# Kernel tuning notes

Hardware: AMD Instinct MI355X
Metric: run time of the kernel (lower is better)

## Reference

```python
import jax, jax.numpy as jnp
import numpy as np

IN_DIM, OUT_DIM = 256, 64
ALPHA = 0.2  # leaky relu negative slope
NEG_INF = -1e30


def setup_inputs() -> dict:
    key = jax.random.key(0)
    k1, k2, k3, k4 = jax.random.split(key, 4)
    B, N = 8, 2048
    h = jax.random.normal(k1, (B, N, IN_DIM), dtype=jnp.float32)
    adj = jax.random.randint(k2, (B, N, N), 0, 2, dtype=jnp.int32)
    # ensure no fully-isolated node (avoids softmax over all -inf)
    idx = jnp.arange(N)
    adj = adj.at[:, idx, idx].set(1)
    # params: fc.weight [out,in] -> store transposed [in,out]; attn_fc.weight [1, 2*out] -> [2*out]
    W = jax.random.normal(k3, (IN_DIM, OUT_DIM), dtype=jnp.float32) / np.sqrt(IN_DIM)
    a = jax.random.normal(k4, (2 * OUT_DIM,), dtype=jnp.float32) / np.sqrt(2 * OUT_DIM)
    return {"h": h, "adj": adj, "W": W, "a": a}


def reference(h, adj, W, a):
    # Wh: [B,N,D]
    Wh = jnp.einsum("bni,io->bno", h, W)
    D = Wh.shape[-1]
    # concat-based additive attention decomposed: e[b,i,j] = lrelu(a1.Wh_i + a2.Wh_j)
    a1, a2 = a[:D], a[D:]
    s1 = Wh @ a1  # [B,N] contribution of row node i
    s2 = Wh @ a2  # [B,N] contribution of col node j
    e = jax.nn.leaky_relu(s1[:, :, None] + s2[:, None, :], negative_slope=ALPHA)  # [B,N,N]
    e = jnp.where(adj == 0, NEG_INF, e)
    attn = jax.nn.softmax(e, axis=-1)
    # dropout is identity in eval mode
    return jnp.einsum("bij,bjd->bid", attn, Wh)
```

## Files before the change

### kernel.cpp

```cpp
#include <hip/hip_runtime.h>
#include <math.h>

#define NB 8
#define NN 2048
#define IN_DIM 256
#define OUT_DIM 64
#define ALPHA 0.2f
#define JSPLIT 8

typedef __attribute__((ext_vector_type(8))) short bf16x8;
typedef __attribute__((ext_vector_type(4))) float f32x4;
typedef __attribute__((ext_vector_type(4))) int i32x4;

__device__ __forceinline__ unsigned short f2bf(float x) {
    union { float f; unsigned u; } v; v.f = x;
    unsigned r = v.u + 0x7FFF + ((v.u >> 16) & 1);
    return (unsigned short)(r >> 16);
}

__device__ __forceinline__ unsigned cvt_pk_bf16(float lo, float hi) {
    unsigned r;
    asm("v_cvt_pk_bf16_f32 %0, %1, %2" : "=v"(r) : "v"(lo), "v"(hi));
    return r;
}

#define WT_STRIDE 264
__global__ __launch_bounds__(256) void wh_kernel(const float* __restrict__ h,
                                                 const float* __restrict__ W,
                                                 const float* __restrict__ a,
                                                 unsigned short* __restrict__ Whbt,
                                                 float* __restrict__ s1,
                                                 float* __restrict__ s2) {
    __shared__ unsigned short Wt[OUT_DIM * WT_STRIDE];
    const int t = threadIdx.x;

    #pragma unroll 8
    for (int rep = 0; rep < 64; ++rep) {
        const int id = rep * 256 + t;
        const int k = id >> 6, n = id & 63;
        Wt[n * WT_STRIDE + k] = f2bf(W[id]);
    }
    __syncthreads();

    const int lane = t & 63, wv = t >> 6;
    const int m = lane & 15, quad = lane >> 4;
    const long gr0 = (long)(blockIdx.x * 4 + wv) * 16;

    f32x4 acc[4];
    #pragma unroll
    for (int nt = 0; nt < 4; ++nt) acc[nt] = (f32x4){0.f, 0.f, 0.f, 0.f};

    #pragma unroll
    for (int ks = 0; ks < 8; ++ks) {
        const int k0 = ks * 32;
        const float* hp = h + (gr0 + m) * IN_DIM + k0 + quad * 8;
        const float4 ha = *(const float4*)hp;
        const float4 hb = *(const float4*)(hp + 4);
        union { bf16x8 v; unsigned u32[4]; } af;
        af.u32[0] = cvt_pk_bf16(ha.x, ha.y);
        af.u32[1] = cvt_pk_bf16(ha.z, ha.w);
        af.u32[2] = cvt_pk_bf16(hb.x, hb.y);
        af.u32[3] = cvt_pk_bf16(hb.z, hb.w);
        #pragma unroll
        for (int nt = 0; nt < 4; ++nt) {
            const bf16x8 bf_ = *(const bf16x8*)(const void*)
                &Wt[(nt * 16 + m) * WT_STRIDE + k0 + quad * 8];
            acc[nt] = __builtin_amdgcn_mfma_f32_16x16x32_bf16(af.v, bf_, acc[nt], 0, 0, 0);
        }
    }

    const int b  = (int)(gr0 >> 11);
    const int ib = (int)(gr0 & 2047);

    #pragma unroll
    for (int nt = 0; nt < 4; ++nt) {
        ushort4 w4;
        w4.x = f2bf(acc[nt][0]); w4.y = f2bf(acc[nt][1]);
        w4.z = f2bf(acc[nt][2]); w4.w = f2bf(acc[nt][3]);
        *(ushort4*)&Whbt[((long)(b * OUT_DIM + nt * 16 + m) << 11) + ib + quad * 4] = w4;
    }

    float a1v[4], a2v[4];
    #pragma unroll
    for (int nt = 0; nt < 4; ++nt) {
        a1v[nt] = a[nt * 16 + m];
        a2v[nt] = a[OUT_DIM + nt * 16 + m];
    }
    #pragma unroll
    for (int reg = 0; reg < 4; ++reg) {
        float p1 = 0.f, p2 = 0.f;
        #pragma unroll
        for (int nt = 0; nt < 4; ++nt) {
            p1 += acc[nt][reg] * a1v[nt];
            p2 += acc[nt][reg] * a2v[nt];
        }
        #pragma unroll
        for (int off = 1; off < 16; off <<= 1) {
            p1 += __shfl_xor(p1, off, 64);
            p2 += __shfl_xor(p2, off, 64);
        }
        if (m == 0) {
            s1[gr0 + quad * 4 + reg] = p1;
            s2[gr0 + quad * 4 + reg] = p2;
        }
    }
}

__global__ __launch_bounds__(256) void attn_kernel(const int* __restrict__ adj,
                                                   const unsigned short* __restrict__ Whbt,
                                                   const float* __restrict__ s1,
                                                   const float* __restrict__ s2,
                                                   float* __restrict__ part,
                                                   float* __restrict__ lpart) {
    const int t = threadIdx.x, lane = t & 63, wv = t >> 6;

    const int bid = blockIdx.x;
    const int js  = bid & (JSPLIT - 1);
    const int itg = (bid >> 3) & 31;
    const int b   = bid >> 8;
    const int i0  = itg * 64 + wv * 16;
    const int jlo = js * (NN / JSPLIT);

    const int m = lane & 15, quad = lane >> 4;

    const float s1v = s1[b * NN + i0 + m];

    f32x4 acc[4];
    #pragma unroll
    for (int nt = 0; nt < 4; ++nt) acc[nt] = (f32x4){0.f, 0.f, 0.f, 0.f};
    float lacc = 0.f;

    const int* adjp = adj + (long)b * NN * NN + (long)(i0 + m) * NN + jlo + quad * 8;
    const float* s2p = s2 + b * NN + jlo + quad * 8;
    const unsigned short* wbase = Whbt + ((long)(b * OUT_DIM) << 11) + jlo + quad * 8;

    i32x4 av0 = __builtin_nontemporal_load((const i32x4*)adjp);
    i32x4 av1 = __builtin_nontemporal_load((const i32x4*)(adjp + 4));
    f32x4 sv0 = *(const f32x4*)s2p;
    f32x4 sv1 = *(const f32x4*)(s2p + 4);

    const int NSTEP = NN / JSPLIT / 32;
    for (int ks = 0; ks < NSTEP; ++ks) {
        const int j0 = ks * 32;

        bf16x8 bfr[4];
        #pragma unroll
        for (int nt = 0; nt < 4; ++nt)
            bfr[nt] = *(const bf16x8*)(const void*)
                &wbase[((long)(nt * 16 + m) << 11) + j0];

        const i32x4 a0 = av0, a1 = av1;
        const f32x4 t0 = sv0, t1 = sv1;
        const int jn = (ks + 1 < NSTEP) ? j0 + 32 : j0;
        av0 = __builtin_nontemporal_load((const i32x4*)(adjp + jn));
        av1 = __builtin_nontemporal_load((const i32x4*)(adjp + jn + 4));
        sv0 = *(const f32x4*)(s2p + jn);
        sv1 = *(const f32x4*)(s2p + jn + 4);

        float p[8];
        #pragma unroll
        for (int u = 0; u < 4; ++u) {
            float e = s1v + t0[u];
            e = fmaxf(e, ALPHA * e);
            const float ex = __expf(e);
            p[u] = (a0[u] != 0) ? ex : 0.f;
        }
        #pragma unroll
        for (int u = 0; u < 4; ++u) {
            float e = s1v + t1[u];
            e = fmaxf(e, ALPHA * e);
            const float ex = __expf(e);
            p[4 + u] = (a1[u] != 0) ? ex : 0.f;
        }
        lacc += ((p[0] + p[1]) + (p[2] + p[3])) + ((p[4] + p[5]) + (p[6] + p[7]));

        union { bf16x8 v; unsigned u32[4]; } af;
        af.u32[0] = cvt_pk_bf16(p[0], p[1]);
        af.u32[1] = cvt_pk_bf16(p[2], p[3]);
        af.u32[2] = cvt_pk_bf16(p[4], p[5]);
        af.u32[3] = cvt_pk_bf16(p[6], p[7]);

        #pragma unroll
        for (int nt = 0; nt < 4; ++nt)
            acc[nt] = __builtin_amdgcn_mfma_f32_16x16x32_bf16(af.v, bfr[nt], acc[nt], 0, 0, 0);
    }

    lacc += __shfl_xor(lacc, 16, 64);
    lacc += __shfl_xor(lacc, 32, 64);
    if (quad == 0)
        lpart[js * (NB * NN) + b * NN + i0 + m] = lacc;

    float* pp = part + (long)js * ((long)NB * NN * OUT_DIM)
                     + ((long)(b * NN + i0) << 6);
    #pragma unroll
    for (int nt = 0; nt < 4; ++nt)
        #pragma unroll
        for (int reg = 0; reg < 4; ++reg)
            pp[(quad * 4 + reg) * OUT_DIM + nt * 16 + m] = acc[nt][reg];
}

__global__ __launch_bounds__(256) void finalize_kernel(const float* __restrict__ part,
                                                       const float* __restrict__ lpart,
                                                       float* __restrict__ out) {
    const int idx = blockIdx.x * 256 + threadIdx.x;
    const int row = idx >> 4;
    float l = 0.f;
    #pragma unroll
    for (int s = 0; s < JSPLIT; ++s) l += lpart[s * (NB * NN) + row];
    float4 v = make_float4(0.f, 0.f, 0.f, 0.f);
    const float4* p4 = (const float4*)part;
    #pragma unroll
    for (int s = 0; s < JSPLIT; ++s) {
        const float4 p = p4[(long)s * ((long)NB * NN * OUT_DIM / 4) + idx];
        v.x += p.x; v.y += p.y; v.z += p.z; v.w += p.w;
    }
    const float inv = 1.f / l;
    v.x *= inv; v.y *= inv; v.z *= inv; v.w *= inv;
    ((float4*)out)[idx] = v;
}

extern "C" void kernel_launch(void* const* d_in, const int* in_sizes, int n_in,
                              void* d_out, int out_size, void* d_ws, size_t ws_size,
                              hipStream_t stream) {
    const float* h   = (const float*)d_in[0];
    const int*   adj = (const int*)d_in[1];
    const float* W   = (const float*)d_in[2];
    const float* a   = (const float*)d_in[3];
    float* out = (float*)d_out;

    float* s1    = (float*)d_ws;
    float* s2    = s1 + NB * NN;
    float* lpart = s2 + NB * NN;
    float* part  = lpart + JSPLIT * NB * NN;
    unsigned short* Whbt = (unsigned short*)(part + (long)JSPLIT * NB * NN * OUT_DIM);

    wh_kernel<<<NB * NN / 64, 256, 0, stream>>>(h, W, a, Whbt, s1, s2);
    attn_kernel<<<NB * (NN / 64) * JSPLIT, 256, 0, stream>>>(adj, Whbt, s1, s2, part, lpart);
    finalize_kernel<<<NB * NN * OUT_DIM / 4 / 256, 256, 0, stream>>>(part, lpart, out);
}
```

Before: 244.0 us.

## Pack adjacency into bitmask in separate pass, halve j-split, prefetch Wh fragments

```diff
diff --git a/kernel.cpp b/kernel.cpp
--- a/kernel.cpp
+++ b/kernel.cpp
@@ -6,11 +6,12 @@
 #define IN_DIM 256
 #define OUT_DIM 64
 #define ALPHA 0.2f
-#define JSPLIT 8
+#define JSPLIT 4
 
 typedef __attribute__((ext_vector_type(8))) short bf16x8;
 typedef __attribute__((ext_vector_type(4))) float f32x4;
 typedef __attribute__((ext_vector_type(4))) int i32x4;
+typedef __attribute__((ext_vector_type(4))) unsigned u32x4;
 
 __device__ __forceinline__ unsigned short f2bf(float x) {
     union { float f; unsigned u; } v; v.f = x;
@@ -22,6 +23,23 @@
     unsigned r;
     asm("v_cvt_pk_bf16_f32 %0, %1, %2" : "=v"(r) : "v"(lo), "v"(hi));
     return r;
+}
+
+__global__ __launch_bounds__(256) void pack_kernel(const int* __restrict__ adj,
+                                                   unsigned* __restrict__ mask) {
+    const int t = threadIdx.x, lane = t & 63, wv = t >> 6;
+    const int r = blockIdx.x * 4 + wv;
+    const int* ap = adj + (long)r * NN + lane * 32;
+    unsigned bits = 0;
+    #pragma unroll
+    for (int u = 0; u < 8; ++u) {
+        const i32x4 v = __builtin_nontemporal_load((const i32x4*)(ap + 4 * u));
+        bits |= (unsigned)(v[0] & 1) << (4 * u + 0);
+        bits |= (unsigned)(v[1] & 1) << (4 * u + 1);
+        bits |= (unsigned)(v[2] & 1) << (4 * u + 2);
+        bits |= (unsigned)(v[3] & 1) << (4 * u + 3);
+    }
+    mask[r * 64 + lane] = bits;
 }
 
 #define WT_STRIDE 264
@@ -106,7 +124,7 @@
     }
 }
 
-__global__ __launch_bounds__(256) void attn_kernel(const int* __restrict__ adj,
+__global__ __launch_bounds__(256) void attn_kernel(const unsigned* __restrict__ mask,
                                                    const unsigned short* __restrict__ Whbt,
                                                    const float* __restrict__ s1,
                                                    const float* __restrict__ s2,
@@ -116,8 +134,8 @@
 
     const int bid = blockIdx.x;
     const int js  = bid & (JSPLIT - 1);
-    const int itg = (bid >> 3) & 31;
-    const int b   = bid >> 8;
+    const int itg = (bid >> 2) & 31;
+    const int b   = bid >> 7;
     const int i0  = itg * 64 + wv * 16;
     const int jlo = js * (NN / JSPLIT);
 
@@ -125,52 +143,54 @@
 
     const float s1v = s1[b * NN + i0 + m];
 
+    const unsigned* mrowp = mask + ((long)(b * NN + i0 + m) << 6) + (js << 4);
+    u32x4 md[4];
+    #pragma unroll
+    for (int d = 0; d < 4; ++d) md[d] = *(const u32x4*)(mrowp + 4 * d);
+
     f32x4 acc[4];
     #pragma unroll
     for (int nt = 0; nt < 4; ++nt) acc[nt] = (f32x4){0.f, 0.f, 0.f, 0.f};
     float lacc = 0.f;
 
-    const int* adjp = adj + (long)b * NN * NN + (long)(i0 + m) * NN + jlo + quad * 8;
     const float* s2p = s2 + b * NN + jlo + quad * 8;
     const unsigned short* wbase = Whbt + ((long)(b * OUT_DIM) << 11) + jlo + quad * 8;
 
-    i32x4 av0 = __builtin_nontemporal_load((const i32x4*)adjp);
-    i32x4 av1 = __builtin_nontemporal_load((const i32x4*)(adjp + 4));
     f32x4 sv0 = *(const f32x4*)s2p;
     f32x4 sv1 = *(const f32x4*)(s2p + 4);
+    bf16x8 bn[4];
+    #pragma unroll
+    for (int nt = 0; nt < 4; ++nt)
+        bn[nt] = *(const bf16x8*)(const void*)&wbase[(long)(nt * 16 + m) << 11];
 
     const int NSTEP = NN / JSPLIT / 32;
+    #pragma unroll
     for (int ks = 0; ks < NSTEP; ++ks) {
         const int j0 = ks * 32;
-
-        bf16x8 bfr[4];
-        #pragma unroll
-        for (int nt = 0; nt < 4; ++nt)
-            bfr[nt] = *(const bf16x8*)(const void*)
-                &wbase[((long)(nt * 16 + m) << 11) + j0];
-
-        const i32x4 a0 = av0, a1 = av1;
+        const int jn = (ks + 1 < NSTEP) ? j0 + 32 : j0;
+
         const f32x4 t0 = sv0, t1 = sv1;
-        const int jn = (ks + 1 < NSTEP) ? j0 + 32 : j0;
-        av0 = __builtin_nontemporal_load((const i32x4*)(adjp + jn));
-        av1 = __builtin_nontemporal_load((const i32x4*)(adjp + jn + 4));
+        bf16x8 bc[4];
+        #pragma unroll
+        for (int nt = 0; nt < 4; ++nt) bc[nt] = bn[nt];
+
         sv0 = *(const f32x4*)(s2p + jn);
         sv1 = *(const f32x4*)(s2p + jn + 4);
+        #pragma unroll
+        for (int nt = 0; nt < 4; ++nt)
+            bn[nt] = *(const bf16x8*)(const void*)
+                &wbase[((long)(nt * 16 + m) << 11) + jn];
+
+        const unsigned mdw  = md[ks >> 2][ks & 3];
+        const unsigned byte8 = (mdw >> (quad * 8)) & 0xffu;
 
         float p[8];
         #pragma unroll
-        for (int u = 0; u < 4; ++u) {
-            float e = s1v + t0[u];
+        for (int u = 0; u < 8; ++u) {
+            float e = s1v + (u < 4 ? t0[u] : t1[u - 4]);
             e = fmaxf(e, ALPHA * e);
             const float ex = __expf(e);
-            p[u] = (a0[u] != 0) ? ex : 0.f;
-        }
-        #pragma unroll
-        for (int u = 0; u < 4; ++u) {
-            float e = s1v + t1[u];
-            e = fmaxf(e, ALPHA * e);
-            const float ex = __expf(e);
-            p[4 + u] = (a1[u] != 0) ? ex : 0.f;
+            p[u] = ((byte8 >> u) & 1u) ? ex : 0.f;
         }
         lacc += ((p[0] + p[1]) + (p[2] + p[3])) + ((p[4] + p[5]) + (p[6] + p[7]));
 
@@ -182,7 +202,7 @@
 
         #pragma unroll
         for (int nt = 0; nt < 4; ++nt)
-            acc[nt] = __builtin_amdgcn_mfma_f32_16x16x32_bf16(af.v, bfr[nt], acc[nt], 0, 0, 0);
+            acc[nt] = __builtin_amdgcn_mfma_f32_16x16x32_bf16(af.v, bc[nt], acc[nt], 0, 0, 0);
     }
 
     lacc += __shfl_xor(lacc, 16, 64);
@@ -233,8 +253,10 @@
     float* lpart = s2 + NB * NN;
     float* part  = lpart + JSPLIT * NB * NN;
     unsigned short* Whbt = (unsigned short*)(part + (long)JSPLIT * NB * NN * OUT_DIM);
-
+    unsigned* mask = (unsigned*)(Whbt + (long)NB * OUT_DIM * NN);
+
+    pack_kernel<<<NB * NN / 4, 256, 0, stream>>>(adj, mask);
     wh_kernel<<<NB * NN / 64, 256, 0, stream>>>(h, W, a, Whbt, s1, s2);
-    attn_kernel<<<NB * (NN / 64) * JSPLIT, 256, 0, stream>>>(adj, Whbt, s1, s2, part, lpart);
+    attn_kernel<<<NB * (NN / 64) * JSPLIT, 256, 0, stream>>>(mask, Whbt, s1, s2, part, lpart);
     finalize_kernel<<<NB * NN * OUT_DIM / 4 / 256, 256, 0, stream>>>(part, lpart, out);
 }
```

Result: slower. 272.1 us (+11.5%).

## Fuse split-J reduction into attention kernel via LDS, drop finalize kernel

Applied to the files above, without the earlier changes.

```diff
diff --git a/kernel.cpp b/kernel.cpp
--- a/kernel.cpp
+++ b/kernel.cpp
@@ -6,7 +6,6 @@
 #define IN_DIM 256
 #define OUT_DIM 64
 #define ALPHA 0.2f
-#define JSPLIT 8
 
 typedef __attribute__((ext_vector_type(8))) short bf16x8;
 typedef __attribute__((ext_vector_type(4))) float f32x4;
@@ -106,20 +105,20 @@
     }
 }
 
+#define AB_STRIDE 68
 __global__ __launch_bounds__(256) void attn_kernel(const int* __restrict__ adj,
                                                    const unsigned short* __restrict__ Whbt,
                                                    const float* __restrict__ s1,
                                                    const float* __restrict__ s2,
-                                                   float* __restrict__ part,
-                                                   float* __restrict__ lpart) {
+                                                   float* __restrict__ out) {
+    __shared__ float accbuf[4][16 * AB_STRIDE];
+    __shared__ float l_lds[4][16];
+
     const int t = threadIdx.x, lane = t & 63, wv = t >> 6;
-
     const int bid = blockIdx.x;
-    const int js  = bid & (JSPLIT - 1);
-    const int itg = (bid >> 3) & 31;
-    const int b   = bid >> 8;
-    const int i0  = itg * 64 + wv * 16;
-    const int jlo = js * (NN / JSPLIT);
+    const int b   = bid >> 7;
+    const int i0  = (bid & 127) * 16;
+    const int jlo = wv * (NN / 4);
 
     const int m = lane & 15, quad = lane >> 4;
 
@@ -138,24 +137,30 @@
     i32x4 av1 = __builtin_nontemporal_load((const i32x4*)(adjp + 4));
     f32x4 sv0 = *(const f32x4*)s2p;
     f32x4 sv1 = *(const f32x4*)(s2p + 4);
-
-    const int NSTEP = NN / JSPLIT / 32;
+    bf16x8 bn[4];
+    #pragma unroll
+    for (int nt = 0; nt < 4; ++nt)
+        bn[nt] = *(const bf16x8*)(const void*)&wbase[(long)(nt * 16 + m) << 11];
+
+    const int NSTEP = NN / 4 / 32;
     for (int ks = 0; ks < NSTEP; ++ks) {
         const int j0 = ks * 32;
-
-        bf16x8 bfr[4];
-        #pragma unroll
-        for (int nt = 0; nt < 4; ++nt)
-            bfr[nt] = *(const bf16x8*)(const void*)
-                &wbase[((long)(nt * 16 + m) << 11) + j0];
+        const int jn = (ks + 1 < NSTEP) ? j0 + 32 : j0;
 
         const i32x4 a0 = av0, a1 = av1;
         const f32x4 t0 = sv0, t1 = sv1;
-        const int jn = (ks + 1 < NSTEP) ? j0 + 32 : j0;
+        bf16x8 bc[4];
+        #pragma unroll
+        for (int nt = 0; nt < 4; ++nt) bc[nt] = bn[nt];
+
         av0 = __builtin_nontemporal_load((const i32x4*)(adjp + jn));
         av1 = __builtin_nontemporal_load((const i32x4*)(adjp + jn + 4));
         sv0 = *(const f32x4*)(s2p + jn);
         sv1 = *(const f32x4*)(s2p + jn + 4);
+        #pragma unroll
+        for (int nt = 0; nt < 4; ++nt)
+            bn[nt] = *(const bf16x8*)(const void*)
+                &wbase[((long)(nt * 16 + m) << 11) + jn];
 
         float p[8];
         #pragma unroll
@@ -182,41 +187,32 @@
 
         #pragma unroll
         for (int nt = 0; nt < 4; ++nt)
-            acc[nt] = __builtin_amdgcn_mfma_f32_16x16x32_bf16(af.v, bfr[nt], acc[nt], 0, 0, 0);
+            acc[nt] = __builtin_amdgcn_mfma_f32_16x16x32_bf16(af.v, bc[nt], acc[nt], 0, 0, 0);
     }
 
     lacc += __shfl_xor(lacc, 16, 64);
     lacc += __shfl_xor(lacc, 32, 64);
-    if (quad == 0)
-        lpart[js * (NB * NN) + b * NN + i0 + m] = lacc;
-
-    float* pp = part + (long)js * ((long)NB * NN * OUT_DIM)
-                     + ((long)(b * NN + i0) << 6);
+    if (quad == 0) l_lds[wv][m] = lacc;
+
     #pragma unroll
     for (int nt = 0; nt < 4; ++nt)
         #pragma unroll
         for (int reg = 0; reg < 4; ++reg)
-            pp[(quad * 4 + reg) * OUT_DIM + nt * 16 + m] = acc[nt][reg];
-}
-
-__global__ __launch_bounds__(256) void finalize_kernel(const float* __restrict__ part,
-                                                       const float* __restrict__ lpart,
-                                                       float* __restrict__ out) {
-    const int idx = blockIdx.x * 256 + threadIdx.x;
-    const int row = idx >> 4;
+            accbuf[wv][(quad * 4 + reg) * AB_STRIDE + nt * 16 + m] = acc[nt][reg];
+
+    __syncthreads();
+
+    const int row = t >> 4, d0 = (t & 15) * 4;
+    f32x4 v = (f32x4){0.f, 0.f, 0.f, 0.f};
     float l = 0.f;
     #pragma unroll
-    for (int s = 0; s < JSPLIT; ++s) l += lpart[s * (NB * NN) + row];
-    float4 v = make_float4(0.f, 0.f, 0.f, 0.f);
-    const float4* p4 = (const float4*)part;
-    #pragma unroll
-    for (int s = 0; s < JSPLIT; ++s) {
-        const float4 p = p4[(long)s * ((long)NB * NN * OUT_DIM / 4) + idx];
-        v.x += p.x; v.y += p.y; v.z += p.z; v.w += p.w;
+    for (int w2 = 0; w2 < 4; ++w2) {
+        v += *(const f32x4*)&accbuf[w2][row * AB_STRIDE + d0];
+        l += l_lds[w2][row];
     }
     const float inv = 1.f / l;
-    v.x *= inv; v.y *= inv; v.z *= inv; v.w *= inv;
-    ((float4*)out)[idx] = v;
+    float4 o; o.x = v[0] * inv; o.y = v[1] * inv; o.z = v[2] * inv; o.w = v[3] * inv;
+    *(float4*)&out[((long)(b * NN + i0 + row) << 6) + d0] = o;
 }
 
 extern "C" void kernel_launch(void* const* d_in, const int* in_sizes, int n_in,
@@ -228,13 +224,10 @@
     const float* a   = (const float*)d_in[3];
     float* out = (float*)d_out;
 
-    float* s1    = (float*)d_ws;
-    float* s2    = s1 + NB * NN;
-    float* lpart = s2 + NB * NN;
-    float* part  = lpart + JSPLIT * NB * NN;
-    unsigned short* Whbt = (unsigned short*)(part + (long)JSPLIT * NB * NN * OUT_DIM);
+    float* s1 = (float*)d_ws;
+    float* s2 = s1 + NB * NN;
+    unsigned short* Whbt = (unsigned short*)(s2 + NB * NN);
 
     wh_kernel<<<NB * NN / 64, 256, 0, stream>>>(h, W, a, Whbt, s1, s2);
-    attn_kernel<<<NB * (NN / 64) * JSPLIT, 256, 0, stream>>>(adj, Whbt, s1, s2, part, lpart);
-    finalize_kernel<<<NB * NN * OUT_DIM / 4 / 256, 256, 0, stream>>>(part, lpart, out);
-}
+    attn_kernel<<<NB * (NN / 16), 256, 0, stream>>>(adj, Whbt, s1, s2, out);
+}
```

Measured after the change: 236.6 us. 3.0% less time.
